# Optimization experiments

Hardware: AMD Instinct MI355X
Metric: run time of the kernel (lower is better)

Reference implementation:

```python
import jax, jax.numpy as jnp
import numpy as np

D_MODEL = 1024
NUM_HEADS = 16
D_K = D_MODEL // NUM_HEADS
NEG_INF = -1e9


def setup_inputs() -> dict:
    key = jax.random.key(0)
    ks = jax.random.split(key, 12)
    B, S = 2, 2048
    Q = jax.random.normal(ks[0], (B, S, D_MODEL), jnp.float32)
    K = jax.random.normal(ks[1], (B, S, D_MODEL), jnp.float32)
    V = jax.random.normal(ks[2], (B, S, D_MODEL), jnp.float32)
    mask = jax.random.randint(ks[3], (B, 1, 1, S), 0, 2, jnp.int32)
    scale = 1.0 / np.sqrt(D_MODEL)
    WQ = jax.random.normal(ks[4], (D_MODEL, D_MODEL), jnp.float32) * scale
    bQ = jnp.zeros((D_MODEL,), jnp.float32)
    WK = jax.random.normal(ks[5], (D_MODEL, D_MODEL), jnp.float32) * scale
    bK = jnp.zeros((D_MODEL,), jnp.float32)
    WV = jax.random.normal(ks[6], (D_MODEL, D_MODEL), jnp.float32) * scale
    bV = jnp.zeros((D_MODEL,), jnp.float32)
    WO = jax.random.normal(ks[7], (D_MODEL, D_MODEL), jnp.float32) * scale
    bO = jnp.zeros((D_MODEL,), jnp.float32)
    return {"Q": Q, "K": K, "V": V, "mask": mask,
            "WQ": WQ, "bQ": bQ, "WK": WK, "bK": bK,
            "WV": WV, "bV": bV, "WO": WO, "bO": bO}


def _split_heads(x):
    # (B, S, d_model) -> (B, H, S, d_k)
    B, S, _ = x.shape
    return x.reshape(B, S, NUM_HEADS, D_K).transpose(0, 2, 1, 3)


def reference(Q, K, V, mask, WQ, bQ, WK, bK, WV, bV, WO, bO):
    B, Sq, _ = Q.shape
    q = _split_heads(Q @ WQ + bQ)   # (B, H, Sq, d_k)
    k = _split_heads(K @ WK + bK)   # (B, H, Sk, d_k)
    v = _split_heads(V @ WV + bV)   # (B, H, Sk, d_v)
    scores = jnp.einsum('bhqd,bhkd->bhqk', q, k) / jnp.sqrt(jnp.float32(D_K))
    scores = jnp.where(mask == 0, jnp.float32(NEG_INF), scores)
    attention = jax.nn.softmax(scores, axis=-1)         # (B, H, Sq, Sk)
    context = jnp.einsum('bhqk,bhkd->bhqd', attention, v)
    context = context.transpose(0, 2, 1, 3).reshape(B, Sq, D_MODEL)
    output = context @ WO + bO
    return (output, attention)
```

## Files before the change

kernel.cpp:

```cpp
#include <hip/hip_runtime.h>

typedef __attribute__((ext_vector_type(8))) __bf16 bf16x8;
typedef __attribute__((ext_vector_type(4))) __bf16 bf16x4;
typedef __attribute__((ext_vector_type(4))) float f32x4;

#define DEVFN static __device__ __forceinline__

#if __has_builtin(__builtin_amdgcn_exp2f)
#define EXP2(x) __builtin_amdgcn_exp2f(x)
#else
#define EXP2(x) exp2f(x)
#endif

DEVFN f32x4 mfma16(bf16x8 a, bf16x8 b, f32x4 c) {
  return __builtin_amdgcn_mfma_f32_16x16x32_bf16(a, b, c, 0, 0, 0);
}

DEVFN void gload16(const void* g, void* l) {
  __builtin_amdgcn_global_load_lds((const __attribute__((address_space(1))) void*)g,
                                   (__attribute__((address_space(3))) void*)l, 16, 0, 0);
}

__global__ __launch_bounds__(256) void transW4(const float* __restrict__ w0,
                                               const float* __restrict__ w1,
                                               const float* __restrict__ w2,
                                               const float* __restrict__ w3,
                                               unsigned short* __restrict__ obase) {
  __shared__ float t[64][65];
  const float* W = blockIdx.z == 0 ? w0 : blockIdx.z == 1 ? w1 : blockIdx.z == 2 ? w2 : w3;
  unsigned short* Wt = obase + ((size_t)blockIdx.z << 20);
  int k0 = blockIdx.x * 64, n0 = blockIdx.y * 64;
  int tid = threadIdx.x;
#pragma unroll
  for (int it = 0; it < 4; ++it) {
    int r = it * 16 + (tid >> 4);
    int c = (tid & 15) * 4;
    float4 v = *(const float4*)(W + (size_t)(k0 + r) * 1024 + n0 + c);
    t[r][c] = v.x; t[r][c + 1] = v.y; t[r][c + 2] = v.z; t[r][c + 3] = v.w;
  }
  __syncthreads();
#pragma unroll
  for (int it = 0; it < 2; ++it) {
    int nl = it * 32 + (tid >> 3);
    int kc = tid & 7;
    bf16x8 o;
#pragma unroll
    for (int j = 0; j < 8; ++j) o[j] = (__bf16)t[kc * 8 + j][nl];
    int n = n0 + nl;
    char* dst = (char*)Wt + (size_t)n * 2048 + (k0 << 1) + ((kc ^ (n & 7)) << 4);
    *(bf16x8*)dst = o;
  }
}

struct GArg {
  const void* A;
  const unsigned short* Bt;
  const float* bias;
  void* out;
  float scale;
};

template <int BM, int BN, int WR, int WC, int AF32, int EPI>
__global__ __launch_bounds__(256, 2) void gemm_t(GArg g0, GArg g1, GArg g2) {
  GArg g = blockIdx.z == 0 ? g0 : blockIdx.z == 1 ? g1 : g2;
  constexpr int MT = BM / WR / 16, NT = BN / WC / 16;
  constexpr int AB = AF32 ? 4 : 2;
  __shared__ char lA[BM * 64 * AB];
  __shared__ char lB[BN * 64 * 2];
  int tid = threadIdx.x, wave = tid >> 6, lane = tid & 63;
  int hi = lane >> 4, lo = lane & 15;
  int m0 = blockIdx.x * BM, n0 = blockIdx.y * BN;
  int wr = wave / WC, wc = wave % WC;
  f32x4 acc[MT][NT];
#pragma unroll
  for (int mt = 0; mt < MT; ++mt)
#pragma unroll
    for (int nt = 0; nt < NT; ++nt) acc[mt][nt] = (f32x4){0.f, 0.f, 0.f, 0.f};

  for (int k0 = 0; k0 < 1024; k0 += 64) {
    if (AF32) {
#pragma unroll
      for (int i = 0; i < BM / 16; ++i) {
        int off = i * 4096 + tid * 16;
        int row = off >> 8, b = off & 255;
        gload16((const char*)g.A + (size_t)(m0 + row) * 4096 + (k0 << 2)
                    + (b ^ ((row & 7) << 4)),
                lA + i * 4096 + wave * 1024);
      }
    } else {
#pragma unroll
      for (int i = 0; i < BM / 32; ++i) {
        int off = i * 4096 + tid * 16;
        int row = off >> 7, b = off & 127;
        gload16((const char*)g.A + (size_t)(m0 + row) * 2048 + (k0 << 1) + b,
                lA + i * 4096 + wave * 1024);
      }
    }
#pragma unroll
    for (int i = 0; i < BN / 32; ++i) {
      int off = i * 4096 + tid * 16;
      int row = off >> 7, b = off & 127;
      gload16((const char*)g.Bt + (size_t)(n0 + row) * 2048 + (k0 << 1) + b,
              lB + i * 4096 + wave * 1024);
    }
    __syncthreads();
#pragma unroll
    for (int kk = 0; kk < 2; ++kk) {
      bf16x8 af[MT], bfr[NT];
#pragma unroll
      for (int mt = 0; mt < MT; ++mt) {
        int row = wr * (BM / WR) + mt * 16 + lo;
        if (AF32) {
          int base = (row << 8) + ((kk << 7) + (hi << 5));
          int sw = (row & 7) << 4;
          f32x4 a0 = *(const f32x4*)(lA + ((base) ^ sw));
          f32x4 a1 = *(const f32x4*)(lA + ((base + 16) ^ sw));
          bf16x8 v;
#pragma unroll
          for (int j = 0; j < 4; ++j) { v[j] = (__bf16)a0[j]; v[4 + j] = (__bf16)a1[j]; }
          af[mt] = v;
        } else {
          int ob = (row << 7) + ((((kk << 2) + hi) << 4) ^ ((row & 7) << 4));
          af[mt] = *(const bf16x8*)(lA + ob);
        }
      }
#pragma unroll
      for (int nt = 0; nt < NT; ++nt) {
        int row = wc * (BN / WC) + nt * 16 + lo;
        int ob = (row << 7) + ((((kk << 2) + hi) << 4) ^ ((row & 7) << 4));
        bfr[nt] = *(const bf16x8*)(lB + ob);
      }
#pragma unroll
      for (int mt = 0; mt < MT; ++mt)
#pragma unroll
        for (int nt = 0; nt < NT; ++nt)
          acc[mt][nt] = mfma16(af[mt], bfr[nt], acc[mt][nt]);
    }
    __syncthreads();
  }

#pragma unroll
  for (int mt = 0; mt < MT; ++mt) {
#pragma unroll
    for (int nt = 0; nt < NT; ++nt) {
      int col = n0 + wc * (BN / WC) + nt * 16 + lo;
      float bs = g.bias[col];
      int row0 = m0 + wr * (BM / WR) + mt * 16 + (hi << 2);
      float vj[4];
#pragma unroll
      for (int j = 0; j < 4; ++j) vj[j] = (acc[mt][nt][j] + bs) * g.scale;
      if (EPI == 1) {
#pragma unroll
        for (int j = 0; j < 4; ++j)
          ((float*)g.out)[(size_t)(row0 + j) * 1024 + col] = vj[j];
      } else if (blockIdx.z == 2) {
        int d = col & 63;
        int bh = (row0 >> 11) * 16 + (col >> 6);
        int s = row0 & 2047;
        bf16x4 o;
#pragma unroll
        for (int j = 0; j < 4; ++j) o[j] = (__bf16)vj[j];
        char* p = (char*)g.out + ((size_t)bh << 18) + (size_t)d * 4096
                  + (s >> 6) * 128 + (((((s & 63) >> 3) ^ (d & 7)) << 4))
                  + ((s & 7) << 1);
        *(bf16x4*)p = o;
      } else {
#pragma unroll
        for (int j = 0; j < 4; ++j) {
          int srow = row0 + j;
          size_t hb = ((size_t)((srow >> 11) * 16 + (col >> 6))) << 18;
          int ib = ((srow & 2047) << 7) + (((col & 63) << 1) ^ ((srow & 7) << 4));
          *(__bf16*)((char*)g.out + hb + ib) = (__bf16)vj[j];
        }
      }
    }
  }
}

__global__ __launch_bounds__(256, 4) void attn_k(
    const unsigned short* __restrict__ qh, const unsigned short* __restrict__ kh,
    const unsigned short* __restrict__ vt, const int* __restrict__ mask,
    float* __restrict__ attn, unsigned short* __restrict__ ctx) {
  constexpr int S = 2048;
  __shared__ unsigned short ktl[64 * 64];
  __shared__ unsigned short vtl[64 * 64];
  __shared__ unsigned long long mkb[32];
  __shared__ float pf[4][16 * 68];

  int tid = threadIdx.x, wave = tid >> 6, lane = tid & 63;
  int hi = lane >> 4, lo = lane & 15;
  int f = blockIdx.y * 32 + blockIdx.x;
  int xcd = f & 7, slot = f >> 3;
  int bh = xcd * 4 + (slot & 3);
  int qb = slot >> 2;
  int b = bh >> 4, h = bh & 15;
  const char* khead = (const char*)kh + ((size_t)bh << 18);
  const char* qhead = (const char*)qh + ((size_t)bh << 18);
  const char* vhead = (const char*)vt + ((size_t)bh << 18);

  for (int it = 0; it < 8; ++it) {
    unsigned long long bal = __ballot(mask[b * S + it * 256 + tid] != 0);
    if (lane == 0) mkb[it * 4 + wave] = bal;
  }
  __syncthreads();

  int q0 = qb * 64 + wave * 16;
  bf16x8 qf[2];
  {
    int row = q0 + lo;
#pragma unroll
    for (int kk = 0; kk < 2; ++kk) {
      int ib = (row << 7) + ((((kk << 2) + hi) << 4) ^ ((row & 7) << 4));
      qf[kk] = *(const bf16x8*)(qhead + ib);
    }
  }

  float lsum[4] = {0.f, 0.f, 0.f, 0.f};

#pragma unroll
  for (int i = 0; i < 2; ++i)
    gload16(khead + i * 4096 + tid * 16, (char*)ktl + i * 4096 + wave * 1024);
  for (int kt = 0; kt < 32; ++kt) {
    const char* cb = (kt & 1) ? (const char*)vtl : (const char*)ktl;
    char* nb = (kt & 1) ? (char*)ktl : (char*)vtl;
    if (kt < 31) {
#pragma unroll
      for (int i = 0; i < 2; ++i)
        gload16(khead + (size_t)(kt + 1) * 8192 + i * 4096 + tid * 16,
                nb + i * 4096 + wave * 1024);
      asm volatile("s_waitcnt vmcnt(2)" ::: "memory");
    } else {
      asm volatile("s_waitcnt vmcnt(0)" ::: "memory");
    }
    __builtin_amdgcn_sched_barrier(0);
    __builtin_amdgcn_s_barrier();
    unsigned long long mw = mkb[kt];
    __builtin_amdgcn_s_setprio(1);
#pragma unroll
    for (int nt = 0; nt < 4; ++nt) {
      int r = nt * 16 + lo;
      f32x4 a = {0.f, 0.f, 0.f, 0.f};
#pragma unroll
      for (int kk = 0; kk < 2; ++kk) {
        int ob = (r << 7) + ((((kk << 2) + hi) << 4) ^ ((r & 7) << 4));
        a = mfma16(qf[kk], *(const bf16x8*)(cb + ob), a);
      }
      bool ok = (mw >> r) & 1ull;
#pragma unroll
      for (int j = 0; j < 4; ++j) lsum[j] += ok ? EXP2(a[j]) : 0.f;
    }
    __builtin_amdgcn_s_setprio(0);
    __builtin_amdgcn_s_barrier();
  }

  float rcp[4];
#pragma unroll
  for (int j = 0; j < 4; ++j) {
    float s = lsum[j];
    s += __shfl_xor(s, 1); s += __shfl_xor(s, 2);
    s += __shfl_xor(s, 4); s += __shfl_xor(s, 8);
    rcp[j] = s > 0.f ? 1.0f / s : 0.f;
  }

  f32x4 cacc[4];
#pragma unroll
  for (int nt = 0; nt < 4; ++nt) cacc[nt] = (f32x4){0.f, 0.f, 0.f, 0.f};

  float* arow = attn + (size_t)bh * S * S;
  float* pfw = pf[wave];

  for (int kt = 0; kt < 32; ++kt) {
#pragma unroll
    for (int i = 0; i < 2; ++i)
      gload16(khead + (size_t)kt * 8192 + i * 4096 + tid * 16,
              (char*)ktl + i * 4096 + wave * 1024);
#pragma unroll
    for (int i = 0; i < 2; ++i) {
      int off = i * 4096 + tid * 16;
      int d = off >> 7, x = off & 127;
      gload16(vhead + (size_t)d * 4096 + kt * 128 + x,
              (char*)vtl + i * 4096 + wave * 1024);
    }
    __syncthreads();
    unsigned long long mw = mkb[kt];
    __builtin_amdgcn_s_setprio(1);
#pragma unroll
    for (int nt = 0; nt < 4; ++nt) {
      int r = nt * 16 + lo;
      f32x4 a = {0.f, 0.f, 0.f, 0.f};
#pragma unroll
      for (int kk = 0; kk < 2; ++kk) {
        int ob = (r << 7) + ((((kk << 2) + hi) << 4) ^ ((r & 7) << 4));
        a = mfma16(qf[kk], *(const bf16x8*)((const char*)ktl + ob), a);
      }
      bool ok = (mw >> r) & 1ull;
#pragma unroll
      for (int j = 0; j < 4; ++j) {
        float pn = ok ? EXP2(a[j]) * rcp[j] : 0.f;
        pfw[((hi << 2) + j) * 68 + r] = pn;
      }
    }
#pragma unroll
    for (int c = 0; c < 2; ++c) {
      f32x4 p0 = *(const f32x4*)&pfw[lo * 68 + c * 32 + hi * 8];
      f32x4 p1 = *(const f32x4*)&pfw[lo * 68 + c * 32 + hi * 8 + 4];
      bf16x8 pa;
#pragma unroll
      for (int i = 0; i < 4; ++i) { pa[i] = (__bf16)p0[i]; pa[4 + i] = (__bf16)p1[i]; }
#pragma unroll
      for (int nt = 0; nt < 4; ++nt) {
        int d = nt * 16 + lo;
        int ob = (d << 7) + ((((c << 2) + hi) << 4) ^ ((d & 7) << 4));
        cacc[nt] = mfma16(pa, *(const bf16x8*)((const char*)vtl + ob), cacc[nt]);
      }
    }
    __builtin_amdgcn_s_setprio(0);
    {
      int rsub = lane >> 4;
      int cb = (lane & 15) << 2;
#pragma unroll
      for (int s = 0; s < 4; ++s) {
        int row = s * 4 + rsub;
        f32x4 v = *(const f32x4*)&pfw[row * 68 + cb];
        __builtin_nontemporal_store(
            v, (f32x4*)(arow + (size_t)(q0 + row) * S + kt * 64 + cb));
      }
    }
    __syncthreads();
  }

#pragma unroll
  for (int nt = 0; nt < 4; ++nt) {
#pragma unroll
    for (int j = 0; j < 4; ++j) {
      int s = q0 + (hi << 2) + j;
      int mrow = b * S + s;
      int n = h * 64 + nt * 16 + lo;
      int ib = (n << 1) ^ ((mrow & 7) << 4);
      *(__bf16*)((char*)ctx + (size_t)mrow * 2048 + ib) = (__bf16)cacc[nt][j];
    }
  }
}

extern "C" void kernel_launch(void* const* d_in, const int* in_sizes, int n_in,
                              void* d_out, int out_size, void* d_ws, size_t ws_size,
                              hipStream_t stream) {
  const float* Q  = (const float*)d_in[0];
  const float* K  = (const float*)d_in[1];
  const float* V  = (const float*)d_in[2];
  const int* mask = (const int*)d_in[3];
  const float* WQ = (const float*)d_in[4];
  const float* bQ = (const float*)d_in[5];
  const float* WK = (const float*)d_in[6];
  const float* bK = (const float*)d_in[7];
  const float* WV = (const float*)d_in[8];
  const float* bV = (const float*)d_in[9];
  const float* WO = (const float*)d_in[10];
  const float* bO = (const float*)d_in[11];

  char* ws = (char*)d_ws;
  const size_t M1 = 1ull << 20;
  unsigned short* WQt = (unsigned short*)(ws + 0 * M1);
  unsigned short* WKt = (unsigned short*)(ws + 2 * M1);
  unsigned short* WVt = (unsigned short*)(ws + 4 * M1);
  unsigned short* WOt = (unsigned short*)(ws + 6 * M1);
  unsigned short* qh  = (unsigned short*)(ws + 8 * M1);
  unsigned short* kh  = (unsigned short*)(ws + 16 * M1);
  unsigned short* vt  = (unsigned short*)(ws + 24 * M1);
  unsigned short* ctx = (unsigned short*)(ws + 32 * M1);

  float* outF = (float*)d_out;
  float* attn = (float*)d_out + 4194304;

  dim3 blk(256);
  const float qscale = 0.125f * 1.44269504088896340736f;

  transW4<<<dim3(16, 16, 4), blk, 0, stream>>>(WQ, WK, WV, WO, WQt);

  GArg aq{Q, WQt, bQ, qh, qscale};
  GArg ak{K, WKt, bK, kh, 1.f};
  GArg av{V, WVt, bV, vt, 1.f};
  gemm_t<128, 128, 2, 2, 1, 0><<<dim3(32, 8, 3), blk, 0, stream>>>(aq, ak, av);

  attn_k<<<dim3(32, 32), blk, 0, stream>>>(qh, kh, vt, mask, attn, ctx);

  GArg ao{ctx, WOt, bO, outF, 1.f};
  gemm_t<64, 128, 1, 4, 0, 1><<<dim3(64, 8, 1), blk, 0, stream>>>(ao, ao, ao);
}
```

Before: 246.4 us.

## Double-buffer K/V tiles in attention pass and move PV MFMA after attn store

The attention kernel now keeps two LDS buffers each for K and V tiles. The second pass prefetches the next tile's K and V with async global-to-LDS loads while computing the current tile, replacing the load-then-syncthreads pattern with vmcnt waits plus barriers. The PV MFMAs are moved after the attention-probability stores so the stores can overlap with compute. LDS use grows, so attn_k occupancy is lowered to 3 and the QKV GEMM's launch bound is raised to 3, which may cause register spills.

```diff
diff --git a/kernel.cpp b/kernel.cpp
--- a/kernel.cpp
+++ b/kernel.cpp
@@ -60,8 +60,8 @@
   float scale;
 };
 
-template <int BM, int BN, int WR, int WC, int AF32, int EPI>
-__global__ __launch_bounds__(256, 2) void gemm_t(GArg g0, GArg g1, GArg g2) {
+template <int BM, int BN, int WR, int WC, int AF32, int EPI, int OCC>
+__global__ __launch_bounds__(256, OCC) void gemm_t(GArg g0, GArg g1, GArg g2) {
   GArg g = blockIdx.z == 0 ? g0 : blockIdx.z == 1 ? g1 : g2;
   constexpr int MT = BM / WR / 16, NT = BN / WC / 16;
   constexpr int AB = AF32 ? 4 : 2;
@@ -177,13 +177,13 @@
   }
 }
 
-__global__ __launch_bounds__(256, 4) void attn_k(
+__global__ __launch_bounds__(256, 3) void attn_k(
     const unsigned short* __restrict__ qh, const unsigned short* __restrict__ kh,
     const unsigned short* __restrict__ vt, const int* __restrict__ mask,
     float* __restrict__ attn, unsigned short* __restrict__ ctx) {
   constexpr int S = 2048;
-  __shared__ unsigned short ktl[64 * 64];
-  __shared__ unsigned short vtl[64 * 64];
+  __shared__ unsigned short ktl[2][64 * 64];
+  __shared__ unsigned short vtl[2][64 * 64];
   __shared__ unsigned long long mkb[32];
   __shared__ float pf[4][16 * 68];
 
@@ -219,15 +219,14 @@
 
 #pragma unroll
   for (int i = 0; i < 2; ++i)
-    gload16(khead + i * 4096 + tid * 16, (char*)ktl + i * 4096 + wave * 1024);
+    gload16(khead + i * 4096 + tid * 16, (char*)ktl[0] + i * 4096 + wave * 1024);
   for (int kt = 0; kt < 32; ++kt) {
-    const char* cb = (kt & 1) ? (const char*)vtl : (const char*)ktl;
-    char* nb = (kt & 1) ? (char*)ktl : (char*)vtl;
+    const char* cb = (const char*)ktl[kt & 1];
     if (kt < 31) {
 #pragma unroll
       for (int i = 0; i < 2; ++i)
         gload16(khead + (size_t)(kt + 1) * 8192 + i * 4096 + tid * 16,
-                nb + i * 4096 + wave * 1024);
+                (char*)ktl[(kt + 1) & 1] + i * 4096 + wave * 1024);
       asm volatile("s_waitcnt vmcnt(2)" ::: "memory");
     } else {
       asm volatile("s_waitcnt vmcnt(0)" ::: "memory");
@@ -250,7 +249,9 @@
       for (int j = 0; j < 4; ++j) lsum[j] += ok ? EXP2(a[j]) : 0.f;
     }
     __builtin_amdgcn_s_setprio(0);
+    __builtin_amdgcn_sched_barrier(0);
     __builtin_amdgcn_s_barrier();
+    __builtin_amdgcn_sched_barrier(0);
   }
 
   float rcp[4];
@@ -269,19 +270,42 @@
   float* arow = attn + (size_t)bh * S * S;
   float* pfw = pf[wave];
 
+#pragma unroll
+  for (int i = 0; i < 2; ++i)
+    gload16(khead + i * 4096 + tid * 16, (char*)ktl[0] + i * 4096 + wave * 1024);
+#pragma unroll
+  for (int i = 0; i < 2; ++i) {
+    int off = i * 4096 + tid * 16;
+    int d = off >> 7, x = off & 127;
+    gload16(vhead + (size_t)d * 4096 + x, (char*)vtl[0] + i * 4096 + wave * 1024);
+  }
+
   for (int kt = 0; kt < 32; ++kt) {
-#pragma unroll
-    for (int i = 0; i < 2; ++i)
-      gload16(khead + (size_t)kt * 8192 + i * 4096 + tid * 16,
-              (char*)ktl + i * 4096 + wave * 1024);
-#pragma unroll
-    for (int i = 0; i < 2; ++i) {
-      int off = i * 4096 + tid * 16;
-      int d = off >> 7, x = off & 127;
-      gload16(vhead + (size_t)d * 4096 + kt * 128 + x,
-              (char*)vtl + i * 4096 + wave * 1024);
-    }
-    __syncthreads();
+    const char* kc = (const char*)ktl[kt & 1];
+    const char* vc = (const char*)vtl[kt & 1];
+    if (kt < 31) {
+      int nb = (kt + 1) & 1;
+#pragma unroll
+      for (int i = 0; i < 2; ++i)
+        gload16(khead + (size_t)(kt + 1) * 8192 + i * 4096 + tid * 16,
+                (char*)ktl[nb] + i * 4096 + wave * 1024);
+#pragma unroll
+      for (int i = 0; i < 2; ++i) {
+        int off = i * 4096 + tid * 16;
+        int d = off >> 7, x = off & 127;
+        gload16(vhead + (size_t)d * 4096 + (kt + 1) * 128 + x,
+                (char*)vtl[nb] + i * 4096 + wave * 1024);
+      }
+    }
+    if (kt == 0 || kt == 31) {
+      asm volatile("s_waitcnt vmcnt(4)" ::: "memory");
+    } else {
+      asm volatile("s_waitcnt vmcnt(8)" ::: "memory");
+    }
+    __builtin_amdgcn_sched_barrier(0);
+    __builtin_amdgcn_s_barrier();
+    __builtin_amdgcn_sched_barrier(0);
+
     unsigned long long mw = mkb[kt];
     __builtin_amdgcn_s_setprio(1);
 #pragma unroll
@@ -291,27 +315,13 @@
 #pragma unroll
       for (int kk = 0; kk < 2; ++kk) {
         int ob = (r << 7) + ((((kk << 2) + hi) << 4) ^ ((r & 7) << 4));
-        a = mfma16(qf[kk], *(const bf16x8*)((const char*)ktl + ob), a);
+        a = mfma16(qf[kk], *(const bf16x8*)(kc + ob), a);
       }
       bool ok = (mw >> r) & 1ull;
 #pragma unroll
       for (int j = 0; j < 4; ++j) {
         float pn = ok ? EXP2(a[j]) * rcp[j] : 0.f;
         pfw[((hi << 2) + j) * 68 + r] = pn;
-      }
-    }
-#pragma unroll
-    for (int c = 0; c < 2; ++c) {
-      f32x4 p0 = *(const f32x4*)&pfw[lo * 68 + c * 32 + hi * 8];
-      f32x4 p1 = *(const f32x4*)&pfw[lo * 68 + c * 32 + hi * 8 + 4];
-      bf16x8 pa;
-#pragma unroll
-      for (int i = 0; i < 4; ++i) { pa[i] = (__bf16)p0[i]; pa[4 + i] = (__bf16)p1[i]; }
-#pragma unroll
-      for (int nt = 0; nt < 4; ++nt) {
-        int d = nt * 16 + lo;
-        int ob = (d << 7) + ((((c << 2) + hi) << 4) ^ ((d & 7) << 4));
-        cacc[nt] = mfma16(pa, *(const bf16x8*)((const char*)vtl + ob), cacc[nt]);
       }
     }
     __builtin_amdgcn_s_setprio(0);
@@ -326,7 +336,25 @@
             v, (f32x4*)(arow + (size_t)(q0 + row) * S + kt * 64 + cb));
       }
     }
-    __syncthreads();
+    __builtin_amdgcn_s_setprio(1);
+#pragma unroll
+    for (int c = 0; c < 2; ++c) {
+      f32x4 p0 = *(const f32x4*)&pfw[lo * 68 + c * 32 + hi * 8];
+      f32x4 p1 = *(const f32x4*)&pfw[lo * 68 + c * 32 + hi * 8 + 4];
+      bf16x8 pa;
+#pragma unroll
+      for (int i = 0; i < 4; ++i) { pa[i] = (__bf16)p0[i]; pa[4 + i] = (__bf16)p1[i]; }
+#pragma unroll
+      for (int nt = 0; nt < 4; ++nt) {
+        int d = nt * 16 + lo;
+        int ob = (d << 7) + ((((c << 2) + hi) << 4) ^ ((d & 7) << 4));
+        cacc[nt] = mfma16(pa, *(const bf16x8*)(vc + ob), cacc[nt]);
+      }
+    }
+    __builtin_amdgcn_s_setprio(0);
+    __builtin_amdgcn_sched_barrier(0);
+    __builtin_amdgcn_s_barrier();
+    __builtin_amdgcn_sched_barrier(0);
   }
 
 #pragma unroll
@@ -380,10 +408,10 @@
   GArg aq{Q, WQt, bQ, qh, qscale};
   GArg ak{K, WKt, bK, kh, 1.f};
   GArg av{V, WVt, bV, vt, 1.f};
-  gemm_t<128, 128, 2, 2, 1, 0><<<dim3(32, 8, 3), blk, 0, stream>>>(aq, ak, av);
+  gemm_t<128, 128, 2, 2, 1, 0, 3><<<dim3(32, 8, 3), blk, 0, stream>>>(aq, ak, av);
 
   attn_k<<<dim3(32, 32), blk, 0, stream>>>(qh, kh, vt, mask, attn, ctx);
 
   GArg ao{ctx, WOt, bO, outF, 1.f};
-  gemm_t<64, 128, 1, 4, 0, 1><<<dim3(64, 8, 1), blk, 0, stream>>>(ao, ao, ao);
-}
+  gemm_t<64, 128, 1, 4, 0, 1, 2><<<dim3(64, 8, 1), blk, 0, stream>>>(ao, ao, ao);
+}
```

After: 247.0 us. Within noise of the previous version (+0.2%).

## Double attention block size to 8 waves and reorder PV after stores

Applied to the files above, without the earlier changes.

Attention blocks now use 512 threads (8 waves, 128 query rows), so each K/V tile loaded into LDS serves twice as many query rows and the grid halves. The PV MFMA step is moved after the nontemporal attention-row stores so stores can overlap with matrix math, and sched barriers are added around the loop barrier. The QKV GEMM gets an occupancy hint of 3 blocks per CU. Larger blocks mean more waves wait at each barrier and fewer blocks are resident per CU.

```diff
diff --git a/kernel.cpp b/kernel.cpp
--- a/kernel.cpp
+++ b/kernel.cpp
@@ -60,8 +60,8 @@
   float scale;
 };
 
-template <int BM, int BN, int WR, int WC, int AF32, int EPI>
-__global__ __launch_bounds__(256, 2) void gemm_t(GArg g0, GArg g1, GArg g2) {
+template <int BM, int BN, int WR, int WC, int AF32, int EPI, int OCC>
+__global__ __launch_bounds__(256, OCC) void gemm_t(GArg g0, GArg g1, GArg g2) {
   GArg g = blockIdx.z == 0 ? g0 : blockIdx.z == 1 ? g1 : g2;
   constexpr int MT = BM / WR / 16, NT = BN / WC / 16;
   constexpr int AB = AF32 ? 4 : 2;
@@ -177,7 +177,7 @@
   }
 }
 
-__global__ __launch_bounds__(256, 4) void attn_k(
+__global__ __launch_bounds__(512, 4) void attn_k(
     const unsigned short* __restrict__ qh, const unsigned short* __restrict__ kh,
     const unsigned short* __restrict__ vt, const int* __restrict__ mask,
     float* __restrict__ attn, unsigned short* __restrict__ ctx) {
@@ -185,11 +185,11 @@
   __shared__ unsigned short ktl[64 * 64];
   __shared__ unsigned short vtl[64 * 64];
   __shared__ unsigned long long mkb[32];
-  __shared__ float pf[4][16 * 68];
+  __shared__ float pf[8][16 * 68];
 
   int tid = threadIdx.x, wave = tid >> 6, lane = tid & 63;
   int hi = lane >> 4, lo = lane & 15;
-  int f = blockIdx.y * 32 + blockIdx.x;
+  int f = blockIdx.y * 16 + blockIdx.x;
   int xcd = f & 7, slot = f >> 3;
   int bh = xcd * 4 + (slot & 3);
   int qb = slot >> 2;
@@ -198,13 +198,13 @@
   const char* qhead = (const char*)qh + ((size_t)bh << 18);
   const char* vhead = (const char*)vt + ((size_t)bh << 18);
 
-  for (int it = 0; it < 8; ++it) {
-    unsigned long long bal = __ballot(mask[b * S + it * 256 + tid] != 0);
-    if (lane == 0) mkb[it * 4 + wave] = bal;
+  for (int it = 0; it < 4; ++it) {
+    unsigned long long bal = __ballot(mask[b * S + it * 512 + tid] != 0);
+    if (lane == 0) mkb[it * 8 + wave] = bal;
   }
   __syncthreads();
 
-  int q0 = qb * 64 + wave * 16;
+  int q0 = qb * 128 + wave * 16;
   bf16x8 qf[2];
   {
     int row = q0 + lo;
@@ -217,18 +217,13 @@
 
   float lsum[4] = {0.f, 0.f, 0.f, 0.f};
 
-#pragma unroll
-  for (int i = 0; i < 2; ++i)
-    gload16(khead + i * 4096 + tid * 16, (char*)ktl + i * 4096 + wave * 1024);
+  gload16(khead + tid * 16, (char*)ktl + wave * 1024);
   for (int kt = 0; kt < 32; ++kt) {
     const char* cb = (kt & 1) ? (const char*)vtl : (const char*)ktl;
     char* nb = (kt & 1) ? (char*)ktl : (char*)vtl;
     if (kt < 31) {
-#pragma unroll
-      for (int i = 0; i < 2; ++i)
-        gload16(khead + (size_t)(kt + 1) * 8192 + i * 4096 + tid * 16,
-                nb + i * 4096 + wave * 1024);
-      asm volatile("s_waitcnt vmcnt(2)" ::: "memory");
+      gload16(khead + (size_t)(kt + 1) * 8192 + tid * 16, nb + wave * 1024);
+      asm volatile("s_waitcnt vmcnt(1)" ::: "memory");
     } else {
       asm volatile("s_waitcnt vmcnt(0)" ::: "memory");
     }
@@ -250,7 +245,9 @@
       for (int j = 0; j < 4; ++j) lsum[j] += ok ? EXP2(a[j]) : 0.f;
     }
     __builtin_amdgcn_s_setprio(0);
+    __builtin_amdgcn_sched_barrier(0);
     __builtin_amdgcn_s_barrier();
+    __builtin_amdgcn_sched_barrier(0);
   }
 
   float rcp[4];
@@ -270,16 +267,10 @@
   float* pfw = pf[wave];
 
   for (int kt = 0; kt < 32; ++kt) {
-#pragma unroll
-    for (int i = 0; i < 2; ++i)
-      gload16(khead + (size_t)kt * 8192 + i * 4096 + tid * 16,
-              (char*)ktl + i * 4096 + wave * 1024);
-#pragma unroll
-    for (int i = 0; i < 2; ++i) {
-      int off = i * 4096 + tid * 16;
-      int d = off >> 7, x = off & 127;
-      gload16(vhead + (size_t)d * 4096 + kt * 128 + x,
-              (char*)vtl + i * 4096 + wave * 1024);
+    gload16(khead + (size_t)kt * 8192 + tid * 16, (char*)ktl + wave * 1024);
+    {
+      int d = tid >> 3, x = (tid & 7) * 16;
+      gload16(vhead + (size_t)d * 4096 + kt * 128 + x, (char*)vtl + wave * 1024);
     }
     __syncthreads();
     unsigned long long mw = mkb[kt];
@@ -298,20 +289,6 @@
       for (int j = 0; j < 4; ++j) {
         float pn = ok ? EXP2(a[j]) * rcp[j] : 0.f;
         pfw[((hi << 2) + j) * 68 + r] = pn;
-      }
-    }
-#pragma unroll
-    for (int c = 0; c < 2; ++c) {
-      f32x4 p0 = *(const f32x4*)&pfw[lo * 68 + c * 32 + hi * 8];
-      f32x4 p1 = *(const f32x4*)&pfw[lo * 68 + c * 32 + hi * 8 + 4];
-      bf16x8 pa;
-#pragma unroll
-      for (int i = 0; i < 4; ++i) { pa[i] = (__bf16)p0[i]; pa[4 + i] = (__bf16)p1[i]; }
-#pragma unroll
-      for (int nt = 0; nt < 4; ++nt) {
-        int d = nt * 16 + lo;
-        int ob = (d << 7) + ((((c << 2) + hi) << 4) ^ ((d & 7) << 4));
-        cacc[nt] = mfma16(pa, *(const bf16x8*)((const char*)vtl + ob), cacc[nt]);
       }
     }
     __builtin_amdgcn_s_setprio(0);
@@ -326,6 +303,22 @@
             v, (f32x4*)(arow + (size_t)(q0 + row) * S + kt * 64 + cb));
       }
     }
+    __builtin_amdgcn_s_setprio(1);
+#pragma unroll
+    for (int c = 0; c < 2; ++c) {
+      f32x4 p0 = *(const f32x4*)&pfw[lo * 68 + c * 32 + hi * 8];
+      f32x4 p1 = *(const f32x4*)&pfw[lo * 68 + c * 32 + hi * 8 + 4];
+      bf16x8 pa;
+#pragma unroll
+      for (int i = 0; i < 4; ++i) { pa[i] = (__bf16)p0[i]; pa[4 + i] = (__bf16)p1[i]; }
+#pragma unroll
+      for (int nt = 0; nt < 4; ++nt) {
+        int d = nt * 16 + lo;
+        int ob = (d << 7) + ((((c << 2) + hi) << 4) ^ ((d & 7) << 4));
+        cacc[nt] = mfma16(pa, *(const bf16x8*)((const char*)vtl + ob), cacc[nt]);
+      }
+    }
+    __builtin_amdgcn_s_setprio(0);
     __syncthreads();
   }
 
@@ -372,18 +365,17 @@
   float* outF = (float*)d_out;
   float* attn = (float*)d_out + 4194304;
 
-  dim3 blk(256);
   const float qscale = 0.125f * 1.44269504088896340736f;
 
-  transW4<<<dim3(16, 16, 4), blk, 0, stream>>>(WQ, WK, WV, WO, WQt);
+  transW4<<<dim3(16, 16, 4), dim3(256), 0, stream>>>(WQ, WK, WV, WO, WQt);
 
   GArg aq{Q, WQt, bQ, qh, qscale};
   GArg ak{K, WKt, bK, kh, 1.f};
   GArg av{V, WVt, bV, vt, 1.f};
-  gemm_t<128, 128, 2, 2, 1, 0><<<dim3(32, 8, 3), blk, 0, stream>>>(aq, ak, av);
-
-  attn_k<<<dim3(32, 32), blk, 0, stream>>>(qh, kh, vt, mask, attn, ctx);
+  gemm_t<128, 128, 2, 2, 1, 0, 3><<<dim3(32, 8, 3), dim3(256), 0, stream>>>(aq, ak, av);
+
+  attn_k<<<dim3(16, 32), dim3(512), 0, stream>>>(qh, kh, vt, mask, attn, ctx);
 
   GArg ao{ctx, WOt, bO, outF, 1.f};
-  gemm_t<64, 128, 1, 4, 0, 1><<<dim3(64, 8, 1), blk, 0, stream>>>(ao, ao, ao);
-}
+  gemm_t<64, 128, 1, 4, 0, 1, 2><<<dim3(64, 8, 1), dim3(256), 0, stream>>>(ao, ao, ao);
+}
```

Result: faster. 225.2 us (-8.6%).
